# Optimization experiments

Hardware: AMD Instinct MI355X
Metric: run time of the kernel (lower is better)

## Reference

```python
import jax, jax.numpy as jnp
import numpy as np
from jax import lax

KSIZE = 3      # match kernel
STRIDE = 1
RATE = 2       # dilation / downscale rate
FUSE_K = 3     # diagonal-fuse kernel
SCALE = 10.0   # softmax scale
FUSE = True
ESC = 1e-4     # escape_NaN, added per-element before the reduce_sum (as in torch code)


def _same_pad(x, k, s):
    # x: [C, H, W] -> zero-padded so that strided k-window 'same' extraction works
    C, H, W = x.shape
    oh, ow = -(-H // s), -(-W // s)
    ph = max(0, (oh - 1) * s + k - H)
    pw = max(0, (ow - 1) * s + k - W)
    xp = jnp.pad(x, ((0, 0), (ph // 2, ph - ph // 2), (pw // 2, pw - pw // 2)))
    return xp, oh, ow


def extract_patches(x, k, s):
    # x: [C, H, W] -> [L, C, k, k], L row-major over output grid (matches torch Unfold)
    C = x.shape[0]
    xp, oh, ow = _same_pad(x, k, s)
    cols = [xp[:, dh:dh + s * (oh - 1) + 1:s, dw:dw + s * (ow - 1) + 1:s]
            for dh in range(k) for dw in range(k)]
    p = jnp.stack(cols, 0).reshape(k, k, C, oh, ow)
    return p.transpose(3, 4, 2, 0, 1).reshape(oh * ow, C, k, k)


def fuse_diag(x):
    # conv with eye(FUSE_K) kernel, 'same' padding: sum of diagonal shifts
    A, B = x.shape
    pt = (FUSE_K - 1) // 2
    pb = FUSE_K - 1 - pt
    xp = jnp.pad(x, ((pt, pb), (pt, pb)))
    out = xp[0:A, 0:B]
    for d in range(1, FUSE_K):
        out = out + xp[d:d + A, d:d + B]
    return out


def _forward(f, b, mask):
    B, C, H, W = f.shape
    kernel = 2 * RATE
    # mask -> mm gate over background patches (shared across batch: torch uses m[0])
    mask_s = mask[0][:, ::4 * RATE, ::4 * RATE]           # [1, H/r, W/r] nearest downsample
    m = extract_patches(mask_s, KSIZE, STRIDE)            # [L, 1, k, k]
    mm = (jnp.mean(m, axis=(1, 2, 3)) == 0.0).astype(f.dtype)[:, None, None]  # [L,1,1]

    def single(fi, bi):
        # raw patches from full-res background for reconstruction: [Lb, C, 2r, 2r]
        raw_w = extract_patches(bi, kernel, RATE * STRIDE)
        # nearest 1/rate downsample
        fs = fi[:, ::RATE, ::RATE]
        bs = bi[:, ::RATE, ::RATE]
        bh, bw = bs.shape[1], bs.shape[2]
        fh, fw = fs.shape[1], fs.shape[2]
        Lb, Lf = bh * bw, fh * fw
        # match patches from downsampled background, L2-normalized per patch
        w = extract_patches(bs, KSIZE, STRIDE)                      # [Lb, C, 3, 3]
        denom = jnp.sqrt(jnp.sum(w * w + ESC, axis=(1, 2, 3), keepdims=True))
        wn = (w / denom).reshape(Lb, -1)                            # [Lb, C*9]
        # correlation = conv of fs with wn filters = patch GEMM
        fp = extract_patches(fs, KSIZE, 1).reshape(Lf, -1)          # [Lf, C*9]
        scores = wn @ fp.T                                          # [Lb, Lf]
        if FUSE:
            s = fuse_diag(scores)
            s = s.reshape(bh, bw, fh, fw).transpose(1, 0, 3, 2).reshape(Lb, Lf)
            s = fuse_diag(s)
            s = s.reshape(bw, bh, fw, fh).transpose(1, 0, 3, 2).reshape(Lb, Lf)
            scores = s
        att = scores.reshape(Lb, fh, fw) * mm
        att = jax.nn.softmax(att * SCALE, axis=0) * mm              # softmax over patches
        # conv_transpose2d(att, raw_w, stride=rate, padding=1) / 4
        rhs = jnp.flip(raw_w, (2, 3)).transpose(1, 0, 2, 3)         # [C, Lb, 2r, 2r] OIHW
        pad = kernel - 1 - 1                                        # k - 1 - torch_padding
        out = lax.conv_general_dilated(
            att[None], rhs, window_strides=(1, 1),
            padding=[(pad, pad), (pad, pad)], lhs_dilation=(RATE, RATE),
            dimension_numbers=('NCHW', 'OIHW', 'NCHW'))[0] / 4.0    # [C, H, W]
        return out

    return jax.vmap(single)(f, b)


def setup_inputs() -> dict:
    key = jax.random.key(0)
    k1, k2 = jax.random.split(key)
    B, C, H, W = 4, 128, 96, 96
    f = jax.random.normal(k1, (B, C, H, W), jnp.float32)
    b = jax.random.normal(k2, (B, C, H, W), jnp.float32)
    mask = jnp.zeros((1, 1, 4 * H, 4 * W), jnp.float32)
    mask = mask.at[:, :, 96:288, 96:288].set(1.0)
    return {"f": f, "b": b, "mask": mask}


def reference(f, b, mask):
    return _forward(f, b, mask)
```

## Files before the change

kernel.cpp:

```cpp
#include <hip/hip_runtime.h>

typedef _Float16 half8 __attribute__((ext_vector_type(8)));
typedef float floatx4 __attribute__((ext_vector_type(4)));

#define LBF 2304
#define K1  1152
#define LDK2 2304

__device__ __forceinline__ void gll16(const _Float16* g, _Float16* l) {
    __builtin_amdgcn_global_load_lds((const __attribute__((address_space(1))) void*)g,
                                     (__attribute__((address_space(3))) void*)l, 16, 0, 0);
}

__device__ __forceinline__ int dec_kc(int s) { return (s >= 0) ? s + 1 : -s - 1; }

__global__ void stage_scan(const float* __restrict__ f, const float* __restrict__ bsrc,
                           const float* __restrict__ mask,
                           float* __restrict__ ds, int* __restrict__ pos) {
    int tid = threadIdx.x;
    if (blockIdx.x < 9216) {
        long flat = (long)blockIdx.x * 256 + tid;
        int p = flat % 2304;
        long rest = flat / 2304;
        int c = rest % 128;
        int b = (rest / 128) % 4;
        int t = rest / (128 * 4);
        int pi = p / 48, pj = p % 48;
        const float* src = t ? bsrc : f;
        ds[flat] = src[(((long)b * 128 + c) * 96 + 2 * pi) * 96 + 2 * pj];
        return;
    }
    int mmb[9], loc[9]; int s = 0;
#pragma unroll
    for (int t = 0; t < 9; t++) {
        int p = tid * 9 + t;
        int pi = p / 48, pj = p % 48;
        float sm = 0.f;
#pragma unroll
        for (int u = 0; u < 3; u++)
#pragma unroll
            for (int v = 0; v < 3; v++) {
                int y = pi - 1 + u, x = pj - 1 + v;
                if ((unsigned)y < 48u && (unsigned)x < 48u)
                    sm += mask[(8 * y) * 384 + 8 * x];
            }
        int m = (sm == 0.f) ? 1 : 0;
        mmb[t] = m; loc[t] = s; s += m;
    }
    __shared__ int sh[256];
    sh[tid] = s; __syncthreads();
    for (int off = 1; off < 256; off <<= 1) {
        int v = (tid >= off) ? sh[tid - off] : 0;
        __syncthreads();
        sh[tid] += v;
        __syncthreads();
    }
    int excl = sh[tid] - s;
#pragma unroll
    for (int t = 0; t < 9; t++) {
        int e = excl + loc[t];
        pos[tid * 9 + t] = mmb[t] ? e : (-e - 1);
    }
}

__global__ void prep_fp(const float* __restrict__ ds, _Float16* __restrict__ fp) {
    int k = blockIdx.x * 128 + threadIdx.x;
    int p = blockIdx.y;
    int b = blockIdx.z;
    int c = k / 9, r = k % 9, u = r / 3, v = r % 3;
    int pi = p / 48, pj = p % 48;
    int y = pi - 1 + u, x = pj - 1 + v;
    float val = 0.f;
    if ((unsigned)y < 48u && (unsigned)x < 48u)
        val = ds[((long)(b * 128 + c)) * 2304 + y * 48 + x];
    fp[((long)b * LBF + p) * K1 + k] = (_Float16)val;
}

__global__ void prep_wn(const float* __restrict__ ds, _Float16* __restrict__ wn) {
    int p = blockIdx.x, b = blockIdx.y;
    int tid = threadIdx.x;
    int pi = p / 48, pj = p % 48;
    const float* dsb = ds + (long)(4 + b) * 128 * 2304;
    float w[9];
    float ss = 0.f;
#pragma unroll
    for (int t = 0; t < 9; t++) {
        int k = tid + t * 128;
        int c = k / 9, r = k % 9, u = r / 3, v = r % 3;
        int y = pi - 1 + u, x = pj - 1 + v;
        float val = 0.f;
        if ((unsigned)y < 48u && (unsigned)x < 48u)
            val = dsb[(long)c * 2304 + y * 48 + x];
        w[t] = val;
        ss += val * val;
    }
    for (int m = 32; m; m >>= 1) ss += __shfl_xor(ss, m);
    __shared__ float sh[2];
    if ((tid & 63) == 0) sh[tid >> 6] = ss;
    __syncthreads();
    float denom = sqrtf(sh[0] + sh[1] + 0.1152f);
    float inv = 1.f / denom;
#pragma unroll
    for (int t = 0; t < 9; t++) {
        int k = tid + t * 128;
        wn[((long)b * LBF + p) * K1 + k] = (_Float16)(w[t] * inv);
    }
}

__global__ void prep_wtc(const float* __restrict__ bsrc, const int* __restrict__ pos,
                         _Float16* __restrict__ wtc) {
    int p = blockIdx.x * 256 + threadIdx.x;
    int c = blockIdx.y;
    int b = blockIdx.z;
    int sp = pos[p];
    long base = ((long)b * 2048 + c * 16) * LDK2;
    if (sp < 0) {
        int kc = dec_kc(pos[2303]);
        int kp = (kc + 63) & ~63;
        int mo = p + sp + 1;
        if (mo < kp - kc) {
#pragma unroll
            for (int n = 0; n < 16; n++)
                wtc[base + (long)n * LDK2 + kc + mo] = (_Float16)0.f;
        }
        return;
    }
    int pi = p / 48, pj = p % 48;
    const float* src = bsrc + ((long)b * 128 + c) * 96 * 96;
#pragma unroll
    for (int u = 0; u < 4; u++) {
        int y = 2 * pi - 1 + u;
        bool yok = (unsigned)y < 96u;
#pragma unroll
        for (int v = 0; v < 4; v++) {
            int x = 2 * pj - 1 + v;
            float val = 0.f;
            if (yok && (unsigned)x < 96u) val = src[y * 96 + x];
            wtc[base + (long)(u * 4 + v) * LDK2 + sp] = (_Float16)val;
        }
    }
}

#define G1_REG 4096

__global__ __launch_bounds__(256)
void gemm1_cv(const _Float16* __restrict__ A, const _Float16* __restrict__ B,
              float* __restrict__ C) {
    __shared__ _Float16 SA[4 * G1_REG];
    __shared__ _Float16 SB[4 * G1_REG];

    int bid = blockIdx.x;
    int wg = (bid & 7) * 162 + (bid >> 3);
    int z = wg / 324; int t = wg - z * 324;
    const int m0 = (t / 18) * 128, n0 = (t % 18) * 128;

    const _Float16* gA = A + (long)z * LBF * K1 + (long)m0 * K1;
    const _Float16* gB = B + (long)z * LBF * K1 + (long)n0 * K1;
    float* Cb = C + (long)z * LBF * LBF;

    const int tid = threadIdx.x;
    const int wave = tid >> 6, lane = tid & 63;
    const int lm = lane & 15, q = lane >> 4;
    const int wm = wave >> 1, wn_ = wave & 1;
    const int soff = (q ^ ((lm >> 1) & 3)) * 8;
    const int srow = lane >> 2;
    const int scol = ((lane & 3) ^ ((lane >> 3) & 3)) * 8;

    floatx4 acc[4][4] = {};

    auto stA = [&](int reg, int kcol) {
        _Float16* dst = SA + reg * G1_REG + wave * 1024;
        gll16(gA + (long)(wave * 32 + srow) * K1 + kcol + scol, dst);
        gll16(gA + (long)(wave * 32 + 16 + srow) * K1 + kcol + scol, dst + 512);
    };
    auto stB = [&](int reg, int kcol) {
        _Float16* dst = SB + reg * G1_REG + wave * 1024;
        gll16(gB + (long)(wave * 32 + srow) * K1 + kcol + scol, dst);
        gll16(gB + (long)(wave * 32 + 16 + srow) * K1 + kcol + scol, dst + 512);
    };
    auto ldA = [&](int reg, int i) -> half8 {
        return *(const half8*)&SA[reg * G1_REG + (wm * 64 + i * 16 + lm) * 32 + soff];
    };
    auto ldB = [&](int reg, int j) -> half8 {
        return *(const half8*)&SB[reg * G1_REG + (wn_ * 64 + j * 16 + lm) * 32 + soff];
    };

    stA(0, 0);  stB(0, 0);
    stA(1, 32); stB(1, 32);
    stA(2, 64); stB(2, 64);
    asm volatile("s_waitcnt vmcnt(8)" ::: "memory");
    __builtin_amdgcn_s_barrier();

    for (int k = 0; k < 18; ++k) {
        const int b = k & 1;
        const int rg0 = b * 2, rg1 = rg0 + 1, og1 = (b ^ 1) * 2 + 1;
        {
            half8 af[4], bf[4];
#pragma unroll
            for (int i = 0; i < 4; ++i) af[i] = ldA(rg0, i);
#pragma unroll
            for (int j = 0; j < 4; ++j) bf[j] = ldB(rg0, j);
            if (k + 1 < 18) {
                int kc = (k + 1) * 64 + 32;
                stA(og1, kc); stB(og1, kc);
                asm volatile("s_waitcnt vmcnt(8) lgkmcnt(0)" ::: "memory");
            } else {
                asm volatile("s_waitcnt vmcnt(0) lgkmcnt(0)" ::: "memory");
            }
            __builtin_amdgcn_s_barrier();
            __builtin_amdgcn_sched_barrier(0);
            __builtin_amdgcn_s_setprio(1);
#pragma unroll
            for (int i = 0; i < 4; ++i)
#pragma unroll
                for (int j = 0; j < 4; ++j)
                    acc[i][j] = __builtin_amdgcn_mfma_f32_16x16x32_f16(af[i], bf[j], acc[i][j], 0, 0, 0);
            __builtin_amdgcn_s_setprio(0);
            __builtin_amdgcn_sched_barrier(0);
            __builtin_amdgcn_s_barrier();
        }
        {
            half8 af[4], bf[4];
#pragma unroll
            for (int i = 0; i < 4; ++i) af[i] = ldA(rg1, i);
#pragma unroll
            for (int j = 0; j < 4; ++j) bf[j] = ldB(rg1, j);
            if (k + 2 < 18) {
                int kc = (k + 2) * 64;
                stA(rg0, kc); stB(rg0, kc);
                asm volatile("s_waitcnt vmcnt(8) lgkmcnt(0)" ::: "memory");
            } else {
                asm volatile("s_waitcnt vmcnt(0) lgkmcnt(0)" ::: "memory");
            }
            __builtin_amdgcn_s_barrier();
            __builtin_amdgcn_sched_barrier(0);
            __builtin_amdgcn_s_setprio(1);
#pragma unroll
            for (int i = 0; i < 4; ++i)
#pragma unroll
                for (int j = 0; j < 4; ++j)
                    acc[i][j] = __builtin_amdgcn_mfma_f32_16x16x32_f16(af[i], bf[j], acc[i][j], 0, 0, 0);
            __builtin_amdgcn_s_setprio(0);
            __builtin_amdgcn_sched_barrier(0);
            __builtin_amdgcn_s_barrier();
        }
    }

    const int col = n0 + wn_ * 64 + lm;
#pragma unroll
    for (int i = 0; i < 4; ++i) {
        const int row = m0 + wm * 64 + i * 16 + q * 4;
#pragma unroll
        for (int j = 0; j < 4; ++j)
#pragma unroll
            for (int r = 0; r < 4; ++r)
                Cb[(long)(row + r) * LBF + col + j * 16] = acc[i][j][r];
    }
}

__device__ __forceinline__ void gemm_compute(const _Float16* lA, const _Float16* lB,
                                             floatx4 (&acc)[4][4],
                                             int wr, int wc, int lm, int pcp) {
    half8 af[4], bf[4];
#pragma unroll
    for (int t = 0; t < 4; t++) {
        af[t] = *(const half8*)&lA[(wr * 64 + t * 16 + lm) * 64 + pcp];
        bf[t] = *(const half8*)&lB[(wc * 64 + t * 16 + lm) * 64 + pcp];
    }
#pragma unroll
    for (int i = 0; i < 4; i++)
#pragma unroll
        for (int j = 0; j < 4; j++)
            acc[i][j] = __builtin_amdgcn_mfma_f32_16x16x32_f16(af[i], bf[j], acc[i][j], 0, 0, 0);
#pragma unroll
    for (int t = 0; t < 4; t++) {
        af[t] = *(const half8*)&lA[(wr * 64 + t * 16 + lm) * 64 + (pcp ^ 32)];
        bf[t] = *(const half8*)&lB[(wc * 64 + t * 16 + lm) * 64 + (pcp ^ 32)];
    }
#pragma unroll
    for (int i = 0; i < 4; i++)
#pragma unroll
        for (int j = 0; j < 4; j++)
            acc[i][j] = __builtin_amdgcn_mfma_f32_16x16x32_f16(af[i], bf[j], acc[i][j], 0, 0, 0);
}

__global__ __launch_bounds__(256)
void gemm_nt64(const _Float16* __restrict__ A, const _Float16* __restrict__ B,
               float* __restrict__ C, int M, int N, int ldk, int swapxy,
               const int* __restrict__ Kpos, int Kstat, long sA, long sB, long sC) {
    A += blockIdx.z * sA; B += blockIdx.z * sB; C += blockIdx.z * sC;
    int K;
    if (Kpos) { int kc = dec_kc(Kpos[0]); K = (kc + 63) & ~63; }
    else K = Kstat;
    const int tid = threadIdx.x;
    const int lane = tid & 63, wave = tid >> 6;
    const int wr = wave >> 1, wc = wave & 1;
    const int bm = swapxy ? blockIdx.x : blockIdx.y;
    const int bn = swapxy ? blockIdx.y : blockIdx.x;
    const int m0 = bm * 128, n0 = bn * 128;

    __shared__ _Float16 sm[4][128 * 64];

    floatx4 acc[4][4] = {};

    const int lm = lane & 15, q = lane >> 4;
    const int pcp = (q ^ (lm & 7)) * 8;

    const int srow8 = lane >> 3;
    const int gc = ((lane & 7) ^ srow8) * 8;
    const _Float16* gA[4]; const _Float16* gB[4];
    int dOff[4];
#pragma unroll
    for (int c = 0; c < 4; c++) {
        int r = (wave * 4 + c) * 8 + srow8;
        gA[c] = A + (long)(m0 + r) * ldk + gc;
        gB[c] = B + (long)(n0 + r) * ldk + gc;
        dOff[c] = (wave * 4 + c) * 512;
    }

    if (K > 0) {
#pragma unroll
        for (int c = 0; c < 4; c++) gll16(gA[c], &sm[0][dOff[c]]);
#pragma unroll
        for (int c = 0; c < 4; c++) gll16(gB[c], &sm[1][dOff[c]]);
        __syncthreads();
        int k0 = 0, buf = 0;
        while (true) {
            int kn = k0 + 64;
            if (kn < K) {
                const int nb = (buf ^ 1) * 2;
#pragma unroll
                for (int c = 0; c < 4; c++) gll16(gA[c] + kn, &sm[nb][dOff[c]]);
#pragma unroll
                for (int c = 0; c < 4; c++) gll16(gB[c] + kn, &sm[nb + 1][dOff[c]]);
            }
            gemm_compute(sm[buf * 2], sm[buf * 2 + 1], acc, wr, wc, lm, pcp);
            __syncthreads();
            k0 = kn; buf ^= 1;
            if (k0 >= K) break;
        }
    }

    const int col = n0 + wc * 64 + lm;
    const int rowq = q * 4;
#pragma unroll
    for (int i = 0; i < 4; i++) {
        int row = m0 + wr * 64 + i * 16 + rowq;
#pragma unroll
        for (int j = 0; j < 4; j++)
#pragma unroll
            for (int r = 0; r < 4; r++)
                C[(long)(row + r) * N + col + j * 16] = acc[i][j][r];
    }
}

__global__ __launch_bounds__(256)
void fuse_sm(const float* __restrict__ ST, const int* __restrict__ pos,
             _Float16* __restrict__ attTc_g) {
    int j = blockIdx.x, bb = blockIdx.y;
    int tid = threadIdx.x;
    const float* S = ST + (long)bb * LBF * LBF;
    _Float16* orow = attTc_g + ((long)bb * LBF + j) * LDK2;
    int Pj = (j % 48) * 48 + j / 48;
    int Rr[3]; bool jok[3];
#pragma unroll
    for (int t = 0; t < 3; t++) {
        int j2 = Pj + t - 1;
        jok[t] = (unsigned)j2 < (unsigned)LBF;
        int jc = jok[t] ? j2 : 0;
        Rr[t] = (jc % 48) * 48 + jc / 48;
    }
    float v[9]; int ps[9];
    float mx = -1e30f;
#pragma unroll
    for (int u = 0; u < 9; u++) {
        int x = tid + u * 256;
        int sp = pos[x];
        ps[u] = sp;
        float xv = 0.f;
        if (sp >= 0) {
            int a = x / 48, b = x - a * 48;
            float acc = 0.f;
#pragma unroll
            for (int t = 0; t < 3; t++) {
                int d2 = t - 1;
                int uu = b * 48 + a + d2;
                if (jok[t] && (unsigned)uu < (unsigned)LBF) {
                    int ad = a + d2;
                    int c = ((unsigned)ad < 48u) ? (x + 48 * d2)
                          : (ad == 48 ? (b + 1) : (2255 + b));
                    int R = Rr[t];
#pragma unroll
                    for (int e = -1; e <= 1; ++e) {
                        int rr = R + e, cc = c + e;
                        if ((unsigned)rr < (unsigned)LBF && (unsigned)cc < (unsigned)LBF)
                            acc += S[(long)rr * LBF + cc];
                    }
                }
            }
            xv = acc * 10.f;
        }
        v[u] = xv;
        mx = fmaxf(mx, xv);
    }
    for (int m = 32; m; m >>= 1) mx = fmaxf(mx, __shfl_xor(mx, m));
    __shared__ float sh[4], sh2[4];
    if ((tid & 63) == 0) sh[tid >> 6] = mx;
    __syncthreads();
    mx = fmaxf(fmaxf(sh[0], sh[1]), fmaxf(sh[2], sh[3]));
    float sum = 0.f;
#pragma unroll
    for (int u = 0; u < 9; u++) { v[u] = __expf(v[u] - mx); sum += v[u]; }
    for (int m = 32; m; m >>= 1) sum += __shfl_xor(sum, m);
    if ((tid & 63) == 0) sh2[tid >> 6] = sum;
    __syncthreads();
    sum = sh2[0] + sh2[1] + sh2[2] + sh2[3];
    float inv = 1.f / sum;
#pragma unroll
    for (int u = 0; u < 9; u++) {
        if (ps[u] >= 0) orow[ps[u]] = (_Float16)(v[u] * inv);
    }
    int kc = dec_kc(pos[2303]);
    int kp = (kc + 63) & ~63;
    if (tid < kp - kc) orow[kc + tid] = (_Float16)0.f;
}

__global__ void scatter_out(const float* __restrict__ MT_, float* __restrict__ out) {
    int yx = blockIdx.x * 256 + threadIdx.x;
    int c = blockIdx.y, b = blockIdx.z;
    int y = yx / 96, x = yx % 96;
    const float* Mb = MT_ + (long)b * 2048 * LBF;
    float s = 0.f;
    for (int uu = (y + 1) & 1; uu < 4; uu += 2) {
        int fi = (y + 1 - uu) >> 1;
        if ((unsigned)fi >= 48u) continue;
        for (int vv = (x + 1) & 1; vv < 4; vv += 2) {
            int fj = (x + 1 - vv) >> 1;
            if ((unsigned)fj >= 48u) continue;
            s += Mb[(long)(c * 16 + uu * 4 + vv) * LBF + fi * 48 + fj];
        }
    }
    out[(((long)b * 128 + c) * 96 + y) * 96 + x] = 0.25f * s;
}

extern "C" void kernel_launch(void* const* d_in, const int* in_sizes, int n_in,
                              void* d_out, int out_size, void* d_ws, size_t ws_size,
                              hipStream_t stream) {
    const float* f    = (const float*)d_in[0];
    const float* bsrc = (const float*)d_in[1];
    const float* mask = (const float*)d_in[2];
    float* out = (float*)d_out;

    char* ws = (char*)d_ws;
    const size_t offR1  = 84934656;
    const size_t offWn  = offR1 + 21233664;
    const size_t offWtc = offR1 + 42467328;
    const size_t offFT1 = offWtc + 37748736;
    const size_t offPos = offFT1 + 2ul * 21233664;
    const size_t NEED   = offPos + 9216;
    if (ws_size < NEED) return;

    float*    ST    = (float*)(ws + 0);
    float*    MT    = (float*)(ws + 0);
    _Float16* fp    = (_Float16*)(ws + offR1);
    _Float16* wn    = (_Float16*)(ws + offWn);
    _Float16* attTc = (_Float16*)(ws + offR1);
    _Float16* Wtc   = (_Float16*)(ws + offWtc);
    float*    ds    = (float*)(ws + offFT1);
    int*      pos   = (int*)(ws + offPos);

    stage_scan<<<dim3(9217), 256, 0, stream>>>(f, bsrc, mask, ds, pos);
    prep_fp<<<dim3(9, 2304, 4), 128, 0, stream>>>(ds, fp);
    prep_wn<<<dim3(2304, 4), 128, 0, stream>>>(ds, wn);
    prep_wtc<<<dim3(9, 128, 4), 256, 0, stream>>>(bsrc, pos, Wtc);

    gemm1_cv<<<dim3(1296), 256, 0, stream>>>(fp, wn, ST);

    fuse_sm<<<dim3(LBF, 4), 256, 0, stream>>>(ST, pos, attTc);

    gemm_nt64<<<dim3(16, 18, 4), 256, 0, stream>>>(Wtc, attTc, MT, 2048, 2304, LDK2, 1,
        pos + 2303, 0, (long)2048 * LDK2, (long)2304 * LDK2, (long)2048 * 2304);

    scatter_out<<<dim3(36, 128, 4), 256, 0, stream>>>(MT, out);
}
```

Before: 484.9 us.

## Split diagonal fuse into two separable passes with intermediate buffer

The single fuse+softmax kernel, which gathered nine scattered score entries per output element, is replaced by two passes. The first pass stages three rows in shared memory, applies the first diagonal shift-sum and writes permuted rows to a scratch buffer. The second pass applies the second diagonal sum with coalesced row reads and then does the softmax. The batch is processed two images at a time so the scratch buffer fits in the reused workspace. This trades scattered global reads for an extra full write and read of the score matrix plus more kernel launches.

```diff
diff --git a/kernel.cpp b/kernel.cpp
--- a/kernel.cpp
+++ b/kernel.cpp
@@ -13,6 +13,8 @@
 }
 
 __device__ __forceinline__ int dec_kc(int s) { return (s >= 0) ? s + 1 : -s - 1; }
+
+__device__ __forceinline__ int permP(int x) { int a = x / 48; return (x - a * 48) * 48 + a; }
 
 __global__ void stage_scan(const float* __restrict__ f, const float* __restrict__ bsrc,
                            const float* __restrict__ mask,
@@ -355,51 +357,64 @@
 }
 
 __global__ __launch_bounds__(256)
-void fuse_sm(const float* __restrict__ ST, const int* __restrict__ pos,
-             _Float16* __restrict__ attTc_g) {
-    int j = blockIdx.x, bb = blockIdx.y;
+void fuse1p(const float* __restrict__ STp, float* __restrict__ G) {
+    int y = blockIdx.x;
+    int slot = blockIdx.y;
+    const float* S = STp + (long)slot * LBF * LBF;
+    float* Grow = G + (long)slot * LBF * LBF + (long)y * LBF;
+
+    int r = permP(y);
+    __shared__ float L[3][LBF];
     int tid = threadIdx.x;
-    const float* S = ST + (long)bb * LBF * LBF;
-    _Float16* orow = attTc_g + ((long)bb * LBF + j) * LDK2;
-    int Pj = (j % 48) * 48 + j / 48;
-    int Rr[3]; bool jok[3];
-#pragma unroll
-    for (int t = 0; t < 3; t++) {
-        int j2 = Pj + t - 1;
-        jok[t] = (unsigned)j2 < (unsigned)LBF;
-        int jc = jok[t] ? j2 : 0;
-        Rr[t] = (jc % 48) * 48 + jc / 48;
-    }
+#pragma unroll
+    for (int s = 0; s < 3; s++) {
+        int rr = r - 1 + s;
+        if ((unsigned)rr < (unsigned)LBF) {
+            const float4* src = (const float4*)(S + (long)rr * LBF);
+            float4* dst = (float4*)L[s];
+            for (int i = tid; i < LBF / 4; i += 256) dst[i] = src[i];
+        }
+    }
+    __syncthreads();
+
+    bool rok0 = (r > 0), rok2 = (r < LBF - 1);
+#pragma unroll
+    for (int u = 0; u < 9; u++) {
+        int m = tid + u * 256;
+        float acc = L[1][m];
+        if (rok0 && m > 0)       acc += L[0][m - 1];
+        if (rok2 && m < LBF - 1) acc += L[2][m + 1];
+        Grow[permP(m)] = acc;
+    }
+}
+
+__global__ __launch_bounds__(256)
+void fuse2sm(const float* __restrict__ G, const int* __restrict__ pos,
+             _Float16* __restrict__ attTcp) {
+    int y0 = blockIdx.x;
+    int slot = blockIdx.y;
+    int tid = threadIdx.x;
+    const float* Gb = G + (long)slot * LBF * LBF;
+    int j = permP(y0);
+    _Float16* orow = attTcp + ((long)slot * LBF + j) * LDK2;
+
+    const float* g0 = Gb + (long)(y0 - 1) * LBF;
+    const float* g1 = Gb + (long)y0 * LBF;
+    const float* g2 = Gb + (long)(y0 + 1) * LBF;
+    bool yok0 = (y0 > 0), yok2 = (y0 < LBF - 1);
+
     float v[9]; int ps[9];
     float mx = -1e30f;
 #pragma unroll
     for (int u = 0; u < 9; u++) {
-        int x = tid + u * 256;
-        int sp = pos[x];
+        int w = tid + u * 256;
+        float a = g1[w];
+        if (yok0 && w > 0)       a += g0[w - 1];
+        if (yok2 && w < LBF - 1) a += g2[w + 1];
+        int i = permP(w);
+        int sp = pos[i];
         ps[u] = sp;
-        float xv = 0.f;
-        if (sp >= 0) {
-            int a = x / 48, b = x - a * 48;
-            float acc = 0.f;
-#pragma unroll
-            for (int t = 0; t < 3; t++) {
-                int d2 = t - 1;
-                int uu = b * 48 + a + d2;
-                if (jok[t] && (unsigned)uu < (unsigned)LBF) {
-                    int ad = a + d2;
-                    int c = ((unsigned)ad < 48u) ? (x + 48 * d2)
-                          : (ad == 48 ? (b + 1) : (2255 + b));
-                    int R = Rr[t];
-#pragma unroll
-                    for (int e = -1; e <= 1; ++e) {
-                        int rr = R + e, cc = c + e;
-                        if ((unsigned)rr < (unsigned)LBF && (unsigned)cc < (unsigned)LBF)
-                            acc += S[(long)rr * LBF + cc];
-                    }
-                }
-            }
-            xv = acc * 10.f;
-        }
+        float xv = (sp >= 0) ? a * 10.f : 0.f;
         v[u] = xv;
         mx = fmaxf(mx, xv);
     }
@@ -467,6 +482,7 @@
     _Float16* attTc = (_Float16*)(ws + offR1);
     _Float16* Wtc   = (_Float16*)(ws + offWtc);
     float*    ds    = (float*)(ws + offFT1);
+    float*    Gbuf  = (float*)(ws + offFT1);
     int*      pos   = (int*)(ws + offPos);
 
     stage_scan<<<dim3(9217), 256, 0, stream>>>(f, bsrc, mask, ds, pos);
@@ -476,7 +492,11 @@
 
     gemm1_cv<<<dim3(1296), 256, 0, stream>>>(fp, wn, ST);
 
-    fuse_sm<<<dim3(LBF, 4), 256, 0, stream>>>(ST, pos, attTc);
+    for (int bb0 = 0; bb0 < 4; bb0 += 2) {
+        fuse1p<<<dim3(LBF, 2), 256, 0, stream>>>(ST + (long)bb0 * LBF * LBF, Gbuf);
+        fuse2sm<<<dim3(LBF, 2), 256, 0, stream>>>(Gbuf, pos,
+            attTc + (long)bb0 * LBF * LDK2);
+    }
 
     gemm_nt64<<<dim3(16, 18, 4), 256, 0, stream>>>(Wtc, attTc, MT, 2048, 2304, LDK2, 1,
         pos + 2303, 0, (long)2048 * LDK2, (long)2304 * LDK2, (long)2048 * 2304);
```

New measurement: 526.0 us. 1.08x slower.

## Split diagonal fuse into separable coalesced pass plus softmax gather

Applied to the files above, without the earlier changes.

The 3x3 diagonal fuse was done entirely inside the softmax kernel, with 9 scattered reads of the score matrix per output. It is now split in two. A first kernel does the first diagonal-shift sum with coalesced float4 row reads into a scratch buffer. The softmax kernel then needs only 3 gathered reads per element. The work is processed in two batch halves so the scratch fits in the existing workspace, at the cost of an extra full-matrix write and read and more kernel launches.

```diff
diff --git a/kernel.cpp b/kernel.cpp
--- a/kernel.cpp
+++ b/kernel.cpp
@@ -355,20 +355,52 @@
 }
 
 __global__ __launch_bounds__(256)
-void fuse_sm(const float* __restrict__ ST, const int* __restrict__ pos,
-             _Float16* __restrict__ attTc_g) {
+void fuseA(const float* __restrict__ ST, float* __restrict__ FT1) {
+    int y = blockIdx.x, bb = blockIdx.y;
+    const float* S = ST + (long)bb * LBF * LBF;
+    float* F = FT1 + (long)bb * LBF * LBF;
+    const float* r0 = S + (long)(y > 0 ? y - 1 : 0) * LBF;
+    const float* r1 = S + (long)y * LBF;
+    const float* r2 = S + (long)(y < LBF - 1 ? y + 1 : y) * LBF;
+    float m0 = (y > 0) ? 1.f : 0.f;
+    float m2 = (y < LBF - 1) ? 1.f : 0.f;
+    float* o = F + (long)y * LBF;
+    int tid = threadIdx.x;
+#pragma unroll
+    for (int u = 0; u < 3; u++) {
+        int qq = tid + u * 256;
+        if (qq < LBF / 4) {
+            int x0 = qq * 4;
+            float4 a = *(const float4*)(r1 + x0);
+            float4 b = *(const float4*)(r0 + x0);
+            float4 c = *(const float4*)(r2 + x0);
+            float lo_m1 = (x0 > 0) ? r0[x0 - 1] : 0.f;
+            float hi_p4 = (x0 + 4 < LBF) ? r2[x0 + 4] : 0.f;
+            float4 out;
+            out.x = a.x + m0 * lo_m1 + m2 * c.y;
+            out.y = a.y + m0 * b.x + m2 * c.z;
+            out.z = a.z + m0 * b.y + m2 * c.w;
+            out.w = a.w + m0 * b.z + m2 * hi_p4;
+            *(float4*)(o + x0) = out;
+        }
+    }
+}
+
+__global__ __launch_bounds__(256)
+void fuseB_softmax(const float* __restrict__ FT1, const int* __restrict__ pos,
+                   _Float16* __restrict__ attTc_g) {
     int j = blockIdx.x, bb = blockIdx.y;
     int tid = threadIdx.x;
-    const float* S = ST + (long)bb * LBF * LBF;
+    const float* F = FT1 + (long)bb * LBF * LBF;
     _Float16* orow = attTc_g + ((long)bb * LBF + j) * LDK2;
     int Pj = (j % 48) * 48 + j / 48;
-    int Rr[3]; bool jok[3];
+    long roff[3]; bool jok[3];
 #pragma unroll
     for (int t = 0; t < 3; t++) {
         int j2 = Pj + t - 1;
         jok[t] = (unsigned)j2 < (unsigned)LBF;
         int jc = jok[t] ? j2 : 0;
-        Rr[t] = (jc % 48) * 48 + jc / 48;
+        roff[t] = (long)((jc % 48) * 48 + jc / 48) * LBF;
     }
     float v[9]; int ps[9];
     float mx = -1e30f;
@@ -380,22 +412,17 @@
         float xv = 0.f;
         if (sp >= 0) {
             int a = x / 48, b = x - a * 48;
+            int Px = b * 48 + a;
             float acc = 0.f;
 #pragma unroll
             for (int t = 0; t < 3; t++) {
                 int d2 = t - 1;
-                int uu = b * 48 + a + d2;
+                int uu = Px + d2;
                 if (jok[t] && (unsigned)uu < (unsigned)LBF) {
                     int ad = a + d2;
                     int c = ((unsigned)ad < 48u) ? (x + 48 * d2)
                           : (ad == 48 ? (b + 1) : (2255 + b));
-                    int R = Rr[t];
-#pragma unroll
-                    for (int e = -1; e <= 1; ++e) {
-                        int rr = R + e, cc = c + e;
-                        if ((unsigned)rr < (unsigned)LBF && (unsigned)cc < (unsigned)LBF)
-                            acc += S[(long)rr * LBF + cc];
-                    }
+                    acc += F[roff[t] + c];
                 }
             }
             xv = acc * 10.f;
@@ -467,6 +494,7 @@
     _Float16* attTc = (_Float16*)(ws + offR1);
     _Float16* Wtc   = (_Float16*)(ws + offWtc);
     float*    ds    = (float*)(ws + offFT1);
+    float*    FT1   = (float*)(ws + offFT1);
     int*      pos   = (int*)(ws + offPos);
 
     stage_scan<<<dim3(9217), 256, 0, stream>>>(f, bsrc, mask, ds, pos);
@@ -476,7 +504,11 @@
 
     gemm1_cv<<<dim3(1296), 256, 0, stream>>>(fp, wn, ST);
 
-    fuse_sm<<<dim3(LBF, 4), 256, 0, stream>>>(ST, pos, attTc);
+    for (int g = 0; g < 2; g++) {
+        fuseA<<<dim3(LBF, 2), 256, 0, stream>>>(ST + (long)g * 2 * LBF * LBF, FT1);
+        fuseB_softmax<<<dim3(LBF, 2), 256, 0, stream>>>(FT1, pos,
+            attTc + (long)g * 2 * LBF * LDK2);
+    }
 
     gemm_nt64<<<dim3(16, 18, 4), 256, 0, stream>>>(Wtc, attTc, MT, 2048, 2304, LDK2, 1,
         pos + 2303, 0, (long)2048 * LDK2, (long)2304 * LDK2, (long)2048 * 2304);
```

Result: faster. 462.0 us (-4.7%).
